# Performance work log

Measured on AMD Instinct MI355X. Metric: run time of the kernel, lower is better.

The kernel has to match this reference:

```python
import jax, jax.numpy as jnp
import numpy as np

TOKENS, HIDDEN, N_EXPERTS = 16384, 2048, 64
JITTER_EPS = 0.01
Z_LOSS_COEFF = 0.001


def setup_inputs() -> dict:
    key = jax.random.key(0)
    k1, k2 = jax.random.split(key)
    x = jax.random.normal(k1, (TOKENS, HIDDEN), dtype=jnp.float32)
    w = jax.random.normal(k2, (N_EXPERTS, HIDDEN), dtype=jnp.float32) * 0.02  # router weight [E,H]
    return {"x": x, "w": w}


def _route_pass(scores_sel, scores, jitter_eps):
    # scores_sel: logits possibly with -inf at already-selected expert (top-2 pass)
    # scores:     original logits (used for abs/clamp factor, as in torch code)
    mx = jnp.max(scores_sel, axis=-1, keepdims=True)                      # [N,1]
    factor = jnp.maximum(jnp.abs(scores), mx)                             # scores.abs().clamp(min=mx)
    mask = jax.lax.stop_gradient((mx - scores) / factor > 2.0 * jitter_eps)
    masked_logits = jnp.where(mask, -jnp.inf, scores_sel)
    # eval path (training=False): selected_experts = argmax of (masked-for-selection) scores
    sel = jnp.argmax(scores_sel, axis=-1)[..., None]                      # [N,1] int
    gates = jax.nn.softmax(masked_logits, axis=-1)
    # mask_for_one: selected == argmax(gates) holds deterministically in eval -> 1.0
    mult = jnp.take_along_axis(gates, sel, axis=-1)                       # [N,1]
    return mult, sel


def reference(x, w):
    logits = x @ w.T                                                      # [N,E]
    # z-loss (identity on logits in forward; scalar returned for completeness)
    z_loss = Z_LOSS_COEFF * jnp.mean(jnp.square(jax.nn.logsumexp(logits, axis=-1)))
    original_gates = jax.nn.softmax(logits, axis=-1)
    # top-1 pass
    m1, s1 = _route_pass(logits, logits, JITTER_EPS)
    # top-2 pass: mask out the first selection
    e_idx = jnp.arange(logits.shape[-1])[None, :]
    scores2 = jnp.where(e_idx == s1, -jnp.inf, logits)
    m2, s2 = _route_pass(scores2, logits, JITTER_EPS)
    multiplier = jnp.concatenate([m1, m2], axis=-1)                       # [N,2]
    selected_experts = jnp.concatenate([s1, s2], axis=-1)                 # [N,2]
    return multiplier, original_gates, selected_experts, z_loss
```

## Files before the change

kernel.cpp:

```cpp
#include <hip/hip_runtime.h>
#include <math.h>

#define TOKENS 16384
#define HIDDEN 2048
#define NEXP   64
#define MT     32
#define KC     64
#define NCHUNK (HIDDEN / KC)
#define NBLK   (TOKENS / MT)

#define GATES_OFF (TOKENS * 2)
#define SEL_OFF   (GATES_OFF + TOKENS * NEXP)
#define Z_OFF     (SEL_OFF + TOKENS * 2)

#define WIMG_BYTES (NEXP * HIDDEN * 2 * 2)

typedef __attribute__((ext_vector_type(8))) _Float16 f16x8;
typedef __attribute__((ext_vector_type(4))) float    f32x4;

__device__ __forceinline__ float wave_sum64(float v) {
    #pragma unroll
    for (int s = 1; s < 64; s <<= 1) v += __shfl_xor(v, s, 64);
    return v;
}

__global__ __launch_bounds__(256) void wconvert(
    const float* __restrict__ w, uint4* __restrict__ wimg)
{
    const int s = blockIdx.x * 256 + threadIdx.x;
    const int c    = s >> 10;
    const int r    = s & 1023;
    const int l    = r & 63;
    const int nt   = (r >> 6) & 1;
    const int kh   = (r >> 7) & 1;
    const int term = (r >> 8) & 1;
    const int eh   = (r >> 9) & 1;
    const int e = eh * 32 + nt * 16 + (l & 15);
    const int k = c * KC + kh * 32 + (l >> 4) * 8;

    const float* src = w + (size_t)e * HIDDEN + k;
    union { _Float16 f[8]; uint4 u; } o;
    #pragma unroll
    for (int j = 0; j < 8; ++j) {
        const float v = src[j];
        const _Float16 h = (_Float16)v;
        o.f[j] = (term == 0) ? h : (_Float16)((v - (float)h) * 4096.f);
    }
    wimg[s] = o.u;
}

__global__ __launch_bounds__(256, 3) void router_main(
    const float* __restrict__ x, const uint4* __restrict__ wimg,
    float* __restrict__ out, float* __restrict__ zpartial)
{
    __shared__ __align__(16) unsigned char lds[16896];
    __shared__ float zred[4];
    unsigned char* ldsA = lds;
    float* lg = (float*)lds;

    const int tid  = threadIdx.x;
    const int wv   = __builtin_amdgcn_readfirstlane(tid >> 6);
    const int lane = tid & 63;
    const int eh   = wv & 1;
    const int kh   = wv >> 1;
    const int t0   = blockIdx.x * MT;

    int xt[2], xq[2], aoff[2];
    #pragma unroll
    for (int p = 0; p < 2; ++p) {
        const int f = tid + 256 * p;
        const int qlo = f & 3, t = (f >> 2) & 31, qhi = f >> 7;
        const int q = qlo + 4 * qhi;
        xt[p] = t; xq[p] = q;
        const int m = t & 15, mt = t >> 4;
        const int ks2 = q >> 3;
        const int lgp = (q >> 1) & 3;
        const int j0  = 4 * (q & 1);
        const int l2  = lgp * 16 + m;
        aoff[p] = (ks2 * 2 + mt) * 1024 + l2 * 16 + j0 * 2;
    }
    const float* xrow0 = x + (size_t)(t0 + xt[0]) * HIDDEN + 4 * xq[0];
    const float* xrow1 = x + (size_t)(t0 + xt[1]) * HIDDEN + 4 * xq[1];

    const uint4* wB = wimg + eh * 512 + kh * 128 + lane;

    const int aro = kh * 2048 + lane * 16;

    f32x4 acc0[2][2], acc1[2][2];
    #pragma unroll
    for (int mt = 0; mt < 2; ++mt)
        #pragma unroll
        for (int nt = 0; nt < 2; ++nt) { acc0[mt][nt] = (f32x4)0.f; acc1[mt][nt] = (f32x4)0.f; }

    {
        const float4 v0 = *(const float4*)(xrow0);
        const float4 v1 = *(const float4*)(xrow1);
        #pragma unroll
        for (int p = 0; p < 2; ++p) {
            const float4 v = p ? v1 : v0;
            union { _Float16 f[4]; uint2 u; } hh, ll;
            #pragma unroll
            for (int j = 0; j < 4; ++j) {
                const float s = (&v.x)[j];
                const _Float16 h = (_Float16)s;
                hh.f[j] = h;
                ll.f[j] = (_Float16)((s - (float)h) * 4096.f);
            }
            *(uint2*)(ldsA + aoff[p])        = hh.u;
            *(uint2*)(ldsA + aoff[p] + 4096) = ll.u;
        }
    }
    float4 xA0 = *(const float4*)(xrow0 + KC);
    float4 xA1 = *(const float4*)(xrow1 + KC);
    f16x8 curB[2][2];
    #pragma unroll
    for (int t = 0; t < 2; ++t)
        #pragma unroll
        for (int n = 0; n < 2; ++n)
            curB[t][n] = *reinterpret_cast<const f16x8*>(wB + t * 256 + n * 64);

    for (int c = 0; c < NCHUNK; ++c) {
        __syncthreads();
        const int cbuf = (c & 1) * 8192;
        const int nbuf = 8192 - cbuf;

        float4 xB0 = xA0, xB1 = xA1;
        if (c + 2 < NCHUNK) {
            xB0 = *(const float4*)(xrow0 + (c + 2) * KC);
            xB1 = *(const float4*)(xrow1 + (c + 2) * KC);
        }
        f16x8 nxtB[2][2];
        #pragma unroll
        for (int t = 0; t < 2; ++t)
            #pragma unroll
            for (int n = 0; n < 2; ++n)
                nxtB[t][n] = (c + 1 < NCHUNK)
                    ? *reinterpret_cast<const f16x8*>(wB + (c + 1) * 1024 + t * 256 + n * 64)
                    : curB[t][n];

        f16x8 Ah[2], Al[2];
        #pragma unroll
        for (int mt = 0; mt < 2; ++mt) {
            Ah[mt] = *(const f16x8*)(ldsA + cbuf + aro + mt * 1024);
            Al[mt] = *(const f16x8*)(ldsA + cbuf + aro + mt * 1024 + 4096);
        }

        if (c + 1 < NCHUNK) {
            #pragma unroll
            for (int p = 0; p < 2; ++p) {
                const float4 v = p ? xA1 : xA0;
                union { _Float16 f[4]; uint2 u; } hh, ll;
                #pragma unroll
                for (int j = 0; j < 4; ++j) {
                    const float s = (&v.x)[j];
                    const _Float16 h = (_Float16)s;
                    hh.f[j] = h;
                    ll.f[j] = (_Float16)((s - (float)h) * 4096.f);
                }
                *(uint2*)(ldsA + nbuf + aoff[p])        = hh.u;
                *(uint2*)(ldsA + nbuf + aoff[p] + 4096) = ll.u;
            }
        }

        #pragma unroll
        for (int mt = 0; mt < 2; ++mt)
            #pragma unroll
            for (int nt = 0; nt < 2; ++nt) {
                acc0[mt][nt] = __builtin_amdgcn_mfma_f32_16x16x32_f16(Ah[mt], curB[0][nt], acc0[mt][nt], 0, 0, 0);
                acc1[mt][nt] = __builtin_amdgcn_mfma_f32_16x16x32_f16(Ah[mt], curB[1][nt], acc1[mt][nt], 0, 0, 0);
                acc1[mt][nt] = __builtin_amdgcn_mfma_f32_16x16x32_f16(Al[mt], curB[0][nt], acc1[mt][nt], 0, 0, 0);
            }

        xA0 = xB0; xA1 = xB1;
        #pragma unroll
        for (int t = 0; t < 2; ++t)
            #pragma unroll
            for (int n = 0; n < 2; ++n)
                curB[t][n] = nxtB[t][n];
    }

    __syncthreads();
    #pragma unroll
    for (int mt = 0; mt < 2; ++mt)
        #pragma unroll
        for (int nt = 0; nt < 2; ++nt)
            #pragma unroll
            for (int r = 0; r < 4; ++r) {
                const int tok = mt * 16 + (lane >> 4) * 4 + r;
                const int e   = eh * 32 + nt * 16 + (lane & 15);
                lg[(kh * 32 + tok) * 66 + e] = acc0[mt][nt][r] + acc1[mt][nt][r] * (1.f / 4096.f);
            }
    __syncthreads();

    float zsum = 0.f;
    for (int tt = 0; tt < 8; ++tt) {
        const int t = wv * 8 + tt;
        const float v = lg[t * 66 + lane] + lg[(32 + t) * 66 + lane];

        float bv = v; int bi = lane;
        #pragma unroll
        for (int s = 1; s < 64; s <<= 1) {
            const float ov = __shfl_xor(bv, s, 64);
            const int   oi = __shfl_xor(bi, s, 64);
            if (ov > bv || (ov == bv && oi < bi)) { bv = ov; bi = oi; }
        }
        const float max1 = bv; const int s1 = bi;

        const float e1 = expf(v - max1);
        const float sume = wave_sum64(e1);
        out[GATES_OFF + (size_t)(t0 + t) * NEXP + lane] = e1 / sume;
        const float lse = max1 + logf(sume);
        zsum += lse * lse;

        const bool mask1 = (max1 - v) > 0.02f * fmaxf(fabsf(v), max1);
        const float sum1 = wave_sum64(mask1 ? 0.f : e1);

        float bv2 = (lane == s1) ? -INFINITY : v; int bi2 = lane;
        #pragma unroll
        for (int s = 1; s < 64; s <<= 1) {
            const float ov = __shfl_xor(bv2, s, 64);
            const int   oi = __shfl_xor(bi2, s, 64);
            if (ov > bv2 || (ov == bv2 && oi < bi2)) { bv2 = ov; bi2 = oi; }
        }
        const float max2 = bv2; const int s2 = bi2;

        const bool mask2 = (max2 - v) > 0.02f * fmaxf(fabsf(v), max2);
        const float p2v = (mask2 || lane == s1) ? 0.f : expf(v - max2);
        const float sum2 = wave_sum64(p2v);

        if (lane == 0) {
            const size_t trow = (size_t)(t0 + t) * 2;
            out[trow + 0] = 1.f / sum1;
            out[trow + 1] = 1.f / sum2;
            out[SEL_OFF + trow + 0] = (float)s1;
            out[SEL_OFF + trow + 1] = (float)s2;
        }
    }

    if (lane == 0) zred[wv] = zsum;
    __syncthreads();
    if (tid == 0)
        zpartial[blockIdx.x] = zred[0] + zred[1] + zred[2] + zred[3];
}

__global__ __launch_bounds__(256) void zfinal(
    const float* __restrict__ zpartial, float* __restrict__ out)
{
    const int tid = threadIdx.x;
    float v = zpartial[tid] + zpartial[tid + 256];
    v = wave_sum64(v);
    __shared__ float red[4];
    if ((tid & 63) == 0) red[tid >> 6] = v;
    __syncthreads();
    if (tid == 0) {
        const float tot = red[0] + red[1] + red[2] + red[3];
        out[Z_OFF] = 0.001f * (tot / (float)TOKENS);
    }
}

extern "C" void kernel_launch(void* const* d_in, const int* in_sizes, int n_in,
                              void* d_out, int out_size, void* d_ws, size_t ws_size,
                              hipStream_t stream) {
    const float* x = (const float*)d_in[0];
    const float* w = (const float*)d_in[1];
    float* out = (float*)d_out;

    uint4* wimg     = (uint4*)d_ws;
    float* zpartial = (float*)((char*)d_ws + WIMG_BYTES);

    wconvert<<<128, 256, 0, stream>>>(w, wimg);
    router_main<<<NBLK, 256, 0, stream>>>(x, wimg, out, zpartial);
    zfinal<<<1, 256, 0, stream>>>(zpartial, out);
}
```

Baseline: 218.8 us.

## Split K across all four waves and load A directly into registers, bypassing LDS

Measured after the change: 218.1 us. About the same (-0.3%).

```diff
diff --git a/kernel.cpp b/kernel.cpp
--- a/kernel.cpp
+++ b/kernel.cpp
@@ -5,8 +5,6 @@
 #define HIDDEN 2048
 #define NEXP   64
 #define MT     32
-#define KC     64
-#define NCHUNK (HIDDEN / KC)
 #define NBLK   (TOKENS / MT)
 
 #define GATES_OFF (TOKENS * 2)
@@ -36,7 +34,7 @@
     const int term = (r >> 8) & 1;
     const int eh   = (r >> 9) & 1;
     const int e = eh * 32 + nt * 16 + (l & 15);
-    const int k = c * KC + kh * 32 + (l >> 4) * 8;
+    const int k = c * 64 + kh * 32 + (l >> 4) * 8;
 
     const float* src = w + (size_t)e * HIDDEN + k;
     union { _Float16 f[8]; uint4 u; } o;
@@ -49,153 +47,125 @@
     wimg[s] = o.u;
 }
 
-__global__ __launch_bounds__(256, 3) void router_main(
+__device__ __forceinline__ void cvt_split(const float4 a, const float4 b,
+                                          f16x8& hi, f16x8& lo) {
+    union { _Float16 f[8]; f16x8 v; } H, L;
+    #pragma unroll
+    for (int j = 0; j < 4; ++j) {
+        const float s0 = (&a.x)[j];
+        const float s1 = (&b.x)[j];
+        const _Float16 h0 = (_Float16)s0;
+        const _Float16 h1 = (_Float16)s1;
+        H.f[j]     = h0;
+        H.f[j + 4] = h1;
+        L.f[j]     = (_Float16)((s0 - (float)h0) * 4096.f);
+        L.f[j + 4] = (_Float16)((s1 - (float)h1) * 4096.f);
+    }
+    hi = H.v; lo = L.v;
+}
+
+struct Pipe {
+    float4 ra0, ra1, ra2, ra3;
+    f16x8  bh[4], bl[4];
+};
+
+__device__ __forceinline__ void loadA(Pipe& P, const float* ax0,
+                                      const float* ax1, int s) {
+    P.ra0 = *(const float4*)(ax0 + s * 32);
+    P.ra1 = *(const float4*)(ax0 + s * 32 + 4);
+    P.ra2 = *(const float4*)(ax1 + s * 32);
+    P.ra3 = *(const float4*)(ax1 + s * 32 + 4);
+}
+
+__device__ __forceinline__ void loadB(Pipe& P, const uint4* wB, int s) {
+    const uint4* p = wB + (s >> 1) * 1024 + (s & 1) * 128;
+    P.bh[0] = *(const f16x8*)(p);
+    P.bh[1] = *(const f16x8*)(p + 64);
+    P.bh[2] = *(const f16x8*)(p + 512);
+    P.bh[3] = *(const f16x8*)(p + 576);
+    P.bl[0] = *(const f16x8*)(p + 256);
+    P.bl[1] = *(const f16x8*)(p + 320);
+    P.bl[2] = *(const f16x8*)(p + 768);
+    P.bl[3] = *(const f16x8*)(p + 832);
+}
+
+__device__ __forceinline__ void domfma(const Pipe& P,
+                                       const f16x8 Ah0, const f16x8 Ah1,
+                                       const f16x8 Al0, const f16x8 Al1,
+                                       f32x4 (&acc0)[2][4], f32x4 (&acc1)[2][4]) {
+    #pragma unroll
+    for (int g = 0; g < 4; ++g) {
+        acc0[0][g] = __builtin_amdgcn_mfma_f32_16x16x32_f16(Ah0, P.bh[g], acc0[0][g], 0, 0, 0);
+        acc1[0][g] = __builtin_amdgcn_mfma_f32_16x16x32_f16(Ah0, P.bl[g], acc1[0][g], 0, 0, 0);
+        acc1[0][g] = __builtin_amdgcn_mfma_f32_16x16x32_f16(Al0, P.bh[g], acc1[0][g], 0, 0, 0);
+        acc0[1][g] = __builtin_amdgcn_mfma_f32_16x16x32_f16(Ah1, P.bh[g], acc0[1][g], 0, 0, 0);
+        acc1[1][g] = __builtin_amdgcn_mfma_f32_16x16x32_f16(Ah1, P.bl[g], acc1[1][g], 0, 0, 0);
+        acc1[1][g] = __builtin_amdgcn_mfma_f32_16x16x32_f16(Al1, P.bh[g], acc1[1][g], 0, 0, 0);
+    }
+}
+
+__global__ __launch_bounds__(256, 2) void router_main(
     const float* __restrict__ x, const uint4* __restrict__ wimg,
     float* __restrict__ out, float* __restrict__ zpartial)
 {
-    __shared__ __align__(16) unsigned char lds[16896];
+    __shared__ __align__(16) float lg[4][32 * 66];
     __shared__ float zred[4];
-    unsigned char* ldsA = lds;
-    float* lg = (float*)lds;
 
     const int tid  = threadIdx.x;
     const int wv   = __builtin_amdgcn_readfirstlane(tid >> 6);
     const int lane = tid & 63;
-    const int eh   = wv & 1;
-    const int kh   = wv >> 1;
     const int t0   = blockIdx.x * MT;
 
-    int xt[2], xq[2], aoff[2];
-    #pragma unroll
-    for (int p = 0; p < 2; ++p) {
-        const int f = tid + 256 * p;
-        const int qlo = f & 3, t = (f >> 2) & 31, qhi = f >> 7;
-        const int q = qlo + 4 * qhi;
-        xt[p] = t; xq[p] = q;
-        const int m = t & 15, mt = t >> 4;
-        const int ks2 = q >> 3;
-        const int lgp = (q >> 1) & 3;
-        const int j0  = 4 * (q & 1);
-        const int l2  = lgp * 16 + m;
-        aoff[p] = (ks2 * 2 + mt) * 1024 + l2 * 16 + j0 * 2;
-    }
-    const float* xrow0 = x + (size_t)(t0 + xt[0]) * HIDDEN + 4 * xq[0];
-    const float* xrow1 = x + (size_t)(t0 + xt[1]) * HIDDEN + 4 * xq[1];
-
-    const uint4* wB = wimg + eh * 512 + kh * 128 + lane;
-
-    const int aro = kh * 2048 + lane * 16;
-
-    f32x4 acc0[2][2], acc1[2][2];
+    const float* ax0 = x + (size_t)(t0 + (lane & 15)) * HIDDEN
+                         + wv * 512 + (lane >> 4) * 8;
+    const float* ax1 = ax0 + 16 * HIDDEN;
+
+    const uint4* wB = wimg + wv * 8192 + lane;
+
+    f32x4 acc0[2][4], acc1[2][4];
     #pragma unroll
     for (int mt = 0; mt < 2; ++mt)
         #pragma unroll
-        for (int nt = 0; nt < 2; ++nt) { acc0[mt][nt] = (f32x4)0.f; acc1[mt][nt] = (f32x4)0.f; }
-
-    {
-        const float4 v0 = *(const float4*)(xrow0);
-        const float4 v1 = *(const float4*)(xrow1);
-        #pragma unroll
-        for (int p = 0; p < 2; ++p) {
-            const float4 v = p ? v1 : v0;
-            union { _Float16 f[4]; uint2 u; } hh, ll;
-            #pragma unroll
-            for (int j = 0; j < 4; ++j) {
-                const float s = (&v.x)[j];
-                const _Float16 h = (_Float16)s;
-                hh.f[j] = h;
-                ll.f[j] = (_Float16)((s - (float)h) * 4096.f);
-            }
-            *(uint2*)(ldsA + aoff[p])        = hh.u;
-            *(uint2*)(ldsA + aoff[p] + 4096) = ll.u;
-        }
-    }
-    float4 xA0 = *(const float4*)(xrow0 + KC);
-    float4 xA1 = *(const float4*)(xrow1 + KC);
-    f16x8 curB[2][2];
-    #pragma unroll
-    for (int t = 0; t < 2; ++t)
-        #pragma unroll
-        for (int n = 0; n < 2; ++n)
-            curB[t][n] = *reinterpret_cast<const f16x8*>(wB + t * 256 + n * 64);
-
-    for (int c = 0; c < NCHUNK; ++c) {
-        __syncthreads();
-        const int cbuf = (c & 1) * 8192;
-        const int nbuf = 8192 - cbuf;
-
-        float4 xB0 = xA0, xB1 = xA1;
-        if (c + 2 < NCHUNK) {
-            xB0 = *(const float4*)(xrow0 + (c + 2) * KC);
-            xB1 = *(const float4*)(xrow1 + (c + 2) * KC);
-        }
-        f16x8 nxtB[2][2];
-        #pragma unroll
-        for (int t = 0; t < 2; ++t)
-            #pragma unroll
-            for (int n = 0; n < 2; ++n)
-                nxtB[t][n] = (c + 1 < NCHUNK)
-                    ? *reinterpret_cast<const f16x8*>(wB + (c + 1) * 1024 + t * 256 + n * 64)
-                    : curB[t][n];
-
-        f16x8 Ah[2], Al[2];
-        #pragma unroll
-        for (int mt = 0; mt < 2; ++mt) {
-            Ah[mt] = *(const f16x8*)(ldsA + cbuf + aro + mt * 1024);
-            Al[mt] = *(const f16x8*)(ldsA + cbuf + aro + mt * 1024 + 4096);
-        }
-
-        if (c + 1 < NCHUNK) {
-            #pragma unroll
-            for (int p = 0; p < 2; ++p) {
-                const float4 v = p ? xA1 : xA0;
-                union { _Float16 f[4]; uint2 u; } hh, ll;
-                #pragma unroll
-                for (int j = 0; j < 4; ++j) {
-                    const float s = (&v.x)[j];
-                    const _Float16 h = (_Float16)s;
-                    hh.f[j] = h;
-                    ll.f[j] = (_Float16)((s - (float)h) * 4096.f);
-                }
-                *(uint2*)(ldsA + nbuf + aoff[p])        = hh.u;
-                *(uint2*)(ldsA + nbuf + aoff[p] + 4096) = ll.u;
-            }
-        }
-
-        #pragma unroll
-        for (int mt = 0; mt < 2; ++mt)
-            #pragma unroll
-            for (int nt = 0; nt < 2; ++nt) {
-                acc0[mt][nt] = __builtin_amdgcn_mfma_f32_16x16x32_f16(Ah[mt], curB[0][nt], acc0[mt][nt], 0, 0, 0);
-                acc1[mt][nt] = __builtin_amdgcn_mfma_f32_16x16x32_f16(Ah[mt], curB[1][nt], acc1[mt][nt], 0, 0, 0);
-                acc1[mt][nt] = __builtin_amdgcn_mfma_f32_16x16x32_f16(Al[mt], curB[0][nt], acc1[mt][nt], 0, 0, 0);
-            }
-
-        xA0 = xB0; xA1 = xB1;
-        #pragma unroll
-        for (int t = 0; t < 2; ++t)
-            #pragma unroll
-            for (int n = 0; n < 2; ++n)
-                curB[t][n] = nxtB[t][n];
-    }
-
-    __syncthreads();
+        for (int g = 0; g < 4; ++g) { acc0[mt][g] = (f32x4)0.f; acc1[mt][g] = (f32x4)0.f; }
+
+    Pipe PA, PB;
+    f16x8 Ah0, Ah1, Al0, Al1;
+
+    loadA(PA, ax0, ax1, 0); loadB(PA, wB, 0);
+    loadA(PB, ax0, ax1, 1); loadB(PB, wB, 1);
+
+    #pragma unroll
+    for (int s = 0; s < 16; s += 2) {
+        cvt_split(PA.ra0, PA.ra1, Ah0, Al0);
+        cvt_split(PA.ra2, PA.ra3, Ah1, Al1);
+        if (s + 2 < 16) loadA(PA, ax0, ax1, s + 2);
+        domfma(PA, Ah0, Ah1, Al0, Al1, acc0, acc1);
+        if (s + 2 < 16) loadB(PA, wB, s + 2);
+
+        cvt_split(PB.ra0, PB.ra1, Ah0, Al0);
+        cvt_split(PB.ra2, PB.ra3, Ah1, Al1);
+        if (s + 3 < 16) loadA(PB, ax0, ax1, s + 3);
+        domfma(PB, Ah0, Ah1, Al0, Al1, acc0, acc1);
+        if (s + 3 < 16) loadB(PB, wB, s + 3);
+    }
+
     #pragma unroll
     for (int mt = 0; mt < 2; ++mt)
         #pragma unroll
-        for (int nt = 0; nt < 2; ++nt)
+        for (int g = 0; g < 4; ++g)
             #pragma unroll
             for (int r = 0; r < 4; ++r) {
                 const int tok = mt * 16 + (lane >> 4) * 4 + r;
-                const int e   = eh * 32 + nt * 16 + (lane & 15);
-                lg[(kh * 32 + tok) * 66 + e] = acc0[mt][nt][r] + acc1[mt][nt][r] * (1.f / 4096.f);
+                const int e   = (g >> 1) * 32 + (g & 1) * 16 + (lane & 15);
+                lg[wv][tok * 66 + e] = acc0[mt][g][r] + acc1[mt][g][r] * (1.f / 4096.f);
             }
     __syncthreads();
 
     float zsum = 0.f;
     for (int tt = 0; tt < 8; ++tt) {
         const int t = wv * 8 + tt;
-        const float v = lg[t * 66 + lane] + lg[(32 + t) * 66 + lane];
+        const int li = t * 66 + lane;
+        const float v = lg[0][li] + lg[1][li] + lg[2][li] + lg[3][li];
 
         float bv = v; int bi = lane;
         #pragma unroll
```
